# Kernel tuning notes

Hardware: AMD Instinct MI355X
Metric: run time of the kernel (lower is better)

The kernel has to match this reference:

```python
import jax, jax.numpy as jnp
import numpy as np

NUM_HEADS = 4

def setup_inputs() -> dict:
    key = jax.random.key(0)
    ks = jax.random.split(key, 8)
    B, C, H, W = 4, 256, 128, 128
    Cq = C // 8  # query/key channels
    x  = jax.random.normal(ks[0], (B, C, H, W), dtype=jnp.float32)
    Wq = jax.random.normal(ks[1], (Cq, C), dtype=jnp.float32) * 0.05
    bq = jax.random.normal(ks[2], (Cq,),  dtype=jnp.float32) * 0.01
    Wk = jax.random.normal(ks[3], (Cq, C), dtype=jnp.float32) * 0.05
    bk = jax.random.normal(ks[4], (Cq,),  dtype=jnp.float32) * 0.01
    Wv = jax.random.normal(ks[5], (C, C),  dtype=jnp.float32) * 0.05
    bv = jax.random.normal(ks[6], (C,),   dtype=jnp.float32) * 0.01
    # torch init is zeros; use a nonzero value so the attention path contributes
    gamma = jnp.array([0.5], dtype=jnp.float32)
    return {"x": x, "Wq": Wq, "bq": bq, "Wk": Wk, "bk": bk, "Wv": Wv, "bv": bv, "gamma": gamma}

def _conv1x1(x, Wm, b):
    # 1x1 conv == per-pixel linear map over channels
    return jnp.einsum('bchw,oc->bohw', x, Wm) + b[None, :, None, None]

def reference(x, Wq, bq, Wk, bk, Wv, bv, gamma):
    B, C, H, W = x.shape
    nh = NUM_HEADS
    # project, then fold heads into batch: (B*nh, c_head, H, W)
    q = _conv1x1(x, Wq, bq).reshape(B * nh, -1, H, W)
    k = _conv1x1(x, Wk, bk).reshape(B * nh, -1, H, W)
    v = _conv1x1(x, Wv, bv).reshape(B * nh, -1, H, W)
    # horizontal (row-wise) attention over W: energy [BH, H, W, W]
    e_h = jnp.einsum('bchw,bchv->bhwv', q, k)
    a_h = jax.nn.softmax(e_h, axis=-1)
    o_h = jnp.einsum('bhwv,bchv->bchw', a_h, v)  # (BH, cv, H, W)
    # vertical (column-wise) attention over H: energy [BH, W, H, H]
    e_v = jnp.einsum('bchw,bcgw->bwhg', q, k)
    a_v = jax.nn.softmax(e_v, axis=-1)
    # original permutes back as (BH, cv, W, H); requires H == W to add
    o_v = jnp.einsum('bwhg,bcgw->bcwh', a_v, v)
    attn = (o_h + o_v).reshape(B, C, H, W)
    return gamma * attn + x
```

## Files before the change

### kernel.cpp

```cpp
#include <hip/hip_runtime.h>

#define HW 16384

typedef __attribute__((ext_vector_type(8))) short short8;
typedef __attribute__((ext_vector_type(16))) float floatx16;
typedef __attribute__((ext_vector_type(4))) unsigned int uvec4;

__device__ inline unsigned short f2bf(float f) {
    unsigned u = __builtin_bit_cast(unsigned, f);
    u = (u + 0x7FFFu + ((u >> 16) & 1u)) >> 16;
    return (unsigned short)u;
}

__device__ inline unsigned pack_bf_trunc(float lo, float hi) {
    return __builtin_amdgcn_perm(__builtin_bit_cast(unsigned, hi),
                                 __builtin_bit_cast(unsigned, lo), 0x07060302u);
}

__global__ __launch_bounds__(256) void cast_xt_kernel(
    const float* __restrict__ x,
    const float* __restrict__ Wq, const float* __restrict__ Wk,
    const float* __restrict__ Wv, unsigned short* __restrict__ Wb,
    unsigned short* __restrict__ xt)
{
    __shared__ unsigned short T[64][66];
    const int tid = threadIdx.x;
    const int p0 = blockIdx.x * 64;
    const int c0 = blockIdx.y * 64;
    const int b  = blockIdx.z;

    if (b == 0 && blockIdx.y == 0 && blockIdx.x < 80) {
        int e0 = (blockIdx.x * 256 + tid) * 4;
        int row = e0 >> 8, col = e0 & 255;
        const float* src = (row < 32) ? (Wq + row * 256 + col)
                         : (row < 64) ? (Wk + (row - 32) * 256 + col)
                                      : (Wv + (row - 64) * 256 + col);
        float4 v = *(const float4*)src;
        if (row < 32) {
            const float L2E = 1.4426950408889634f;
            v.x *= L2E; v.y *= L2E; v.z *= L2E; v.w *= L2E;
        }
        uint2 pk;
        pk.x = f2bf(v.x) | ((unsigned)f2bf(v.y) << 16);
        pk.y = f2bf(v.z) | ((unsigned)f2bf(v.w) << 16);
        *(uint2*)&Wb[e0] = pk;
    }

    #pragma unroll
    for (int i = 0; i < 4; i++) {
        int e = i * 256 + tid;
        int c = e >> 4, seg = e & 15;
        float4 v = *(const float4*)&x[((b * 256 + c0 + c) << 14) + p0 + seg * 4];
        ((unsigned*)&T[c][seg * 4])[0] = f2bf(v.x) | ((unsigned)f2bf(v.y) << 16);
        ((unsigned*)&T[c][seg * 4])[1] = f2bf(v.z) | ((unsigned)f2bf(v.w) << 16);
    }
    __syncthreads();
    #pragma unroll
    for (int i = 0; i < 2; i++) {
        int e = i * 256 + tid;
        int p = e >> 3, cs = e & 7;
        unsigned short t[8];
        #pragma unroll
        for (int j = 0; j < 8; j++) t[j] = T[cs * 8 + j][p];
        uint4 pk;
        pk.x = t[0] | ((unsigned)t[1] << 16);
        pk.y = t[2] | ((unsigned)t[3] << 16);
        pk.z = t[4] | ((unsigned)t[5] << 16);
        pk.w = t[6] | ((unsigned)t[7] << 16);
        *(uint4*)&xt[(((b << 14) + p0 + p) << 8) + c0 + cs * 8] = pk;
    }
}

__global__ __launch_bounds__(256, 3) void proj_mfma_kernel(
    const unsigned short* __restrict__ Wb, const unsigned short* __restrict__ xt,
    const float* __restrict__ bq, const float* __restrict__ bk,
    const float* __restrict__ bv,
    unsigned short* __restrict__ qb, unsigned short* __restrict__ kb,
    unsigned short* __restrict__ vb)
{
    __shared__ __align__(16) unsigned short As[64 * 64];
    __shared__ __align__(16) unsigned short Bs[256 * 64];
    __shared__ float biasS[64];
    const int tid = threadIdx.x;
    const int logical = (blockIdx.x & 7) * 160 + (blockIdx.x >> 3);
    const int y5 = logical % 5;
    const int pb = logical / 5;
    const int p0  = (pb & 63) * 256;
    const int oc0 = y5 * 64;
    const int b   = pb >> 6;
    const int w = tid >> 6, lr = tid & 31, lh = (tid & 63) >> 5;

    if (tid < 64) biasS[tid] = (oc0 == 0)
        ? ((tid < 32) ? bq[tid] * 1.4426950408889634f : bk[tid - 32])
        : bv[oc0 - 64 + tid];

    floatx16 z16 = {0,0,0,0,0,0,0,0,0,0,0,0,0,0,0,0};
    floatx16 acc[2][2] = {{z16, z16}, {z16, z16}};
    const int bpx = (b << 14) + p0;

    for (int kc = 0; kc < 256; kc += 64) {
        if (kc) __syncthreads();
        #pragma unroll
        for (int i = 0; i < 2; i++) {
            int e = i * 256 + tid;
            int row = e >> 3, seg = e & 7, cp = seg ^ (row & 7);
            *(uint4*)&As[row * 64 + cp * 8] =
                *(const uint4*)&Wb[(oc0 + row) * 256 + kc + seg * 8];
        }
        #pragma unroll
        for (int i = 0; i < 8; i++) {
            int e = i * 256 + tid;
            int row = e >> 3, seg = e & 7, cp = seg ^ (row & 7);
            *(uint4*)&Bs[row * 64 + cp * 8] =
                *(const uint4*)&xt[((bpx + row) << 8) + kc + seg * 8];
        }
        __syncthreads();
        #pragma unroll
        for (int ks = 0; ks < 4; ks++) {
            int c = 2 * ks + lh;
            int cx = (c ^ (lr & 7)) * 8;
            short8 af0 = *(const short8*)&As[lr * 64 + cx];
            short8 af1 = *(const short8*)&As[(32 + lr) * 64 + cx];
            short8 bf0 = *(const short8*)&Bs[(64 * w + lr) * 64 + cx];
            short8 bf1 = *(const short8*)&Bs[(64 * w + 32 + lr) * 64 + cx];
            acc[0][0] = __builtin_amdgcn_mfma_f32_32x32x16_bf16(af0, bf0, acc[0][0], 0, 0, 0);
            acc[0][1] = __builtin_amdgcn_mfma_f32_32x32x16_bf16(af0, bf1, acc[0][1], 0, 0, 0);
            acc[1][0] = __builtin_amdgcn_mfma_f32_32x32x16_bf16(af1, bf0, acc[1][0], 0, 0, 0);
            acc[1][1] = __builtin_amdgcn_mfma_f32_32x32x16_bf16(af1, bf1, acc[1][1], 0, 0, 0);
        }
    }

    __syncthreads();
    if (oc0 == 0) {
        unsigned short* Cq = Bs;
        #pragma unroll
        for (int i = 0; i < 2; i++) {
            #pragma unroll
            for (int j = 0; j < 2; j++) {
                int px = 64 * w + 32 * j + lr;
                #pragma unroll
                for (int g = 0; g < 4; g++) {
                    float v0 = acc[i][j][4*g+0] + biasS[32*i + 8*g + 4*lh + 0];
                    float v1 = acc[i][j][4*g+1] + biasS[32*i + 8*g + 4*lh + 1];
                    float v2 = acc[i][j][4*g+2] + biasS[32*i + 8*g + 4*lh + 2];
                    float v3 = acc[i][j][4*g+3] + biasS[32*i + 8*g + 4*lh + 3];
                    uint2 u; u.x = pack_bf_trunc(v0, v1); u.y = pack_bf_trunc(v2, v3);
                    int cp = (4 * i + g) ^ (px & 7);
                    *(uint2*)&Cq[px * 64 + cp * 8 + 4 * lh] = u;
                }
            }
        }
        __syncthreads();
        #pragma unroll
        for (int i = 0; i < 8; i++) {
            int px = tid;
            int cp = i ^ (px & 7);
            uint4 val = *(const uint4*)&Cq[px * 64 + cp * 8];
            if (i < 4) *(uint4*)&qb[(unsigned)((b * 4 + i)     * HW + p0 + px) * 8] = val;
            else       *(uint4*)&kb[(unsigned)((b * 4 + i - 4) * HW + p0 + px) * 8] = val;
        }
    } else {
        unsigned short* Cv = Bs;
        #pragma unroll
        for (int i = 0; i < 2; i++) {
            #pragma unroll
            for (int j = 0; j < 2; j++) {
                int px = 64 * w + 32 * j + lr;
                #pragma unroll
                for (int reg = 0; reg < 16; reg++) {
                    int oc = 32 * i + (reg & 3) + 8 * (reg >> 2) + 4 * lh;
                    float v = acc[i][j][reg] + biasS[oc];
                    int cp = (px >> 3) ^ (oc & 31);
                    Cv[oc * 256 + cp * 8 + (px & 7)] =
                        (unsigned short)(__builtin_bit_cast(unsigned, v) >> 16);
                }
            }
        }
        __syncthreads();
        #pragma unroll
        for (int i = 0; i < 8; i++) {
            int u = i * 256 + tid;
            int oc = u >> 5, seg = u & 31;
            int cp = seg ^ (oc & 31);
            uint4 val = *(const uint4*)&Cv[oc * 256 + cp * 8];
            *(uint4*)&vb[(unsigned)(b * 256 + oc0 - 64 + oc) * HW + p0 + seg * 8] = val;
        }
    }
}

__global__ __launch_bounds__(256) void tv_kernel(
    const unsigned short* __restrict__ vb, unsigned short* __restrict__ vt)
{
    __shared__ unsigned short T[64][66];
    const int plane = blockIdx.y;
    const int tile  = blockIdx.x;
    const int tx = tile & 1, ty = tile >> 1;
    const unsigned* src = (const unsigned*)(vb + plane * HW);
    unsigned*       dst = (unsigned*)(vt + plane * HW);
    const int tid = threadIdx.x;
    #pragma unroll
    for (int i = 0; i < 8; i++) {
        int e = i * 256 + tid;
        int r = e >> 5, cp = e & 31;
        *(unsigned*)&T[r][2 * cp] = src[(ty * 64 + r) * 64 + tx * 32 + cp];
    }
    __syncthreads();
    #pragma unroll
    for (int i = 0; i < 8; i++) {
        int e = i * 256 + tid;
        int c = e >> 5, rp = e & 31;
        unsigned lo = T[2 * rp][c], hi = T[2 * rp + 1][c];
        dst[(tx * 64 + c) * 64 + ty * 32 + rp] = lo | (hi << 16);
    }
}

__global__ __launch_bounds__(256, 2) void attn_kernel(
    const unsigned short* __restrict__ qb, const unsigned short* __restrict__ kb,
    const unsigned short* __restrict__ vb,
    const unsigned short* __restrict__ vt,
    const float* __restrict__ xin, const float* __restrict__ gamma,
    float* __restrict__ out)
{
    __shared__ __align__(16) unsigned short Vs[2][64 * 128];

    const int tid = threadIdx.x;
    const int logical = (blockIdx.x & 7) * 256 + (blockIdx.x >> 3);
    const int y = logical & 127, bh = logical >> 7;
    const int w = tid >> 6, l = tid & 63, lr = l & 31, lh = l >> 5;

    #pragma unroll
    for (int s = 0; s < 2; s++) {
        const unsigned short* vsrc = s ? vt : vb;
        #pragma unroll
        for (int i = 0; i < 4; i++) {
            int e = i * 256 + tid;
            int ch = e >> 4, sg = e & 15, sgp = sg ^ (ch & 15);
            *(uint4*)&Vs[s][ch * 128 + sgp * 8] =
                *(const uint4*)(vsrc + (bh * 64 + ch) * HW + y * 128 + sg * 8);
        }
    }
    __syncthreads();

    floatx16 z16 = {0,0,0,0,0,0,0,0,0,0,0,0,0,0,0,0};
    floatx16 oh0 = z16, oh1 = z16;
    floatx16 ov0 = z16, ov1 = z16;
    short8 z8 = {0,0,0,0,0,0,0,0};
    float ssA = 1.0f, ssB = 1.0f;

    const unsigned short* qpl = qb + bh * (HW * 8);
    const unsigned short* kpl = kb + bh * (HW * 8);

    #pragma unroll
    for (int stage = 0; stage < 2; stage++) {
        short8 bf = z8;
        if (lh == 0) {
            int px = 32 * w + lr;
            int off = stage ? (px * 128 + y) : (y * 128 + px);
            bf = *(const short8*)(qpl + off * 8);
        }

        floatx16 et[4];
        #pragma unroll
        for (int kg = 0; kg < 4; kg++) {
            short8 af = z8;
            if (lh == 0) {
                int px = 32 * kg + lr;
                int off = stage ? (px * 128 + y) : (y * 128 + px);
                af = *(const short8*)(kpl + off * 8);
            }
            et[kg] = __builtin_amdgcn_mfma_f32_32x32x16_bf16(af, bf, z16, 0, 0, 0);
        }

        float partial = 0.f;
        #pragma unroll
        for (int kg = 0; kg < 4; kg++) {
            floatx16 e = et[kg];
            #pragma unroll
            for (int r = 0; r < 16; r++) {
                float p = exp2f(e[r]);
                e[r] = p;
                partial += p;
            }
            #pragma unroll
            for (int cc = 0; cc < 2; cc++) {
                unsigned X0 = pack_bf_trunc(e[8*cc+0], e[8*cc+1]);
                unsigned X1 = pack_bf_trunc(e[8*cc+2], e[8*cc+3]);
                unsigned X2 = pack_bf_trunc(e[8*cc+4], e[8*cc+5]);
                unsigned X3 = pack_bf_trunc(e[8*cc+6], e[8*cc+7]);
                unsigned pX0 = __shfl_xor(X0, 32);
                unsigned pX1 = __shfl_xor(X1, 32);
                unsigned pX2 = __shfl_xor(X2, 32);
                unsigned pX3 = __shfl_xor(X3, 32);
                uvec4 t;
                t.x = lh ? pX2 : X0;
                t.y = lh ? pX3 : X1;
                t.z = lh ? X2  : pX0;
                t.w = lh ? X3  : pX1;
                short8 pf = __builtin_bit_cast(short8, t);
                int ks = 2 * kg + cc;
                int cp = ((2 * ks + lh) ^ (lr & 15)) * 8;
                short8 v0 = *(const short8*)&Vs[stage][lr * 128 + cp];
                short8 v1 = *(const short8*)&Vs[stage][(32 + lr) * 128 + cp];
                if (stage == 0) {
                    oh0 = __builtin_amdgcn_mfma_f32_32x32x16_bf16(v0, pf, oh0, 0, 0, 0);
                    oh1 = __builtin_amdgcn_mfma_f32_32x32x16_bf16(v1, pf, oh1, 0, 0, 0);
                } else {
                    ov0 = __builtin_amdgcn_mfma_f32_32x32x16_bf16(v0, pf, ov0, 0, 0, 0);
                    ov1 = __builtin_amdgcn_mfma_f32_32x32x16_bf16(v1, pf, ov1, 0, 0, 0);
                }
            }
        }
        float ssum = partial + __shfl_xor(partial, 32);
        if (stage == 0) ssA = ssum; else ssB = ssum;
    }

    __syncthreads();

    const float g  = gamma[0];
    const float g0 = g / ssA, g1 = g / ssB;
    const int xq = 32 * w + lr;
    #pragma unroll
    for (int reg = 0; reg < 16; reg++) {
        int ch = (reg & 3) + 8 * (reg >> 2) + 4 * lh;
        int idx0 = (bh * 64 + ch) * HW + y * 128 + xq;
        int idx1 = (bh * 64 + 32 + ch) * HW + y * 128 + xq;
        out[idx0] = g0 * oh0[reg] + g1 * ov0[reg] + xin[idx0];
        out[idx1] = g0 * oh1[reg] + g1 * ov1[reg] + xin[idx1];
    }
}

extern "C" void kernel_launch(void* const* d_in, const int* in_sizes, int n_in,
                              void* d_out, int out_size, void* d_ws, size_t ws_size,
                              hipStream_t stream) {
    const float* x     = (const float*)d_in[0];
    const float* Wq    = (const float*)d_in[1];
    const float* bq    = (const float*)d_in[2];
    const float* Wk    = (const float*)d_in[3];
    const float* bk    = (const float*)d_in[4];
    const float* Wv    = (const float*)d_in[5];
    const float* bv    = (const float*)d_in[6];
    const float* gamma = (const float*)d_in[7];
    float* out = (float*)d_out;

    unsigned short* Wb   = (unsigned short*)d_ws;
    unsigned short* qb16 = Wb + 320 * 256;
    unsigned short* kb16 = qb16 + 16 * HW * 8;
    unsigned short* qt16 = kb16 + 16 * HW * 8;
    unsigned short* kt16 = qt16 + 16 * HW * 8;
    unsigned short* vb16 = kt16 + 16 * HW * 8;
    unsigned short* vt16 = vb16 + 1024 * HW;
    unsigned short* xt = (unsigned short*)d_out;
    (void)qt16; (void)kt16;

    cast_xt_kernel<<<dim3(256, 4, 4), 256, 0, stream>>>(x, Wq, Wk, Wv, Wb, xt);
    proj_mfma_kernel<<<dim3(1280), 256, 0, stream>>>(Wb, xt, bq, bk, bv, qb16, kb16, vb16);
    tv_kernel<<<dim3(4, 1024), 256, 0, stream>>>(vb16, vt16);
    attn_kernel<<<dim3(2048), 256, 0, stream>>>(qb16, kb16, vb16, vt16, x, gamma, out);
}
```

Measured before the change: 199.8 us.

## Fuse QKV projection and transpose into attention kernel, recomputing per row/column

After: 249.3 us. 24.8% more time.

```diff
diff --git a/kernel.cpp b/kernel.cpp
--- a/kernel.cpp
+++ b/kernel.cpp
@@ -15,6 +15,10 @@
 __device__ inline unsigned pack_bf_trunc(float lo, float hi) {
     return __builtin_amdgcn_perm(__builtin_bit_cast(unsigned, hi),
                                  __builtin_bit_cast(unsigned, lo), 0x07060302u);
+}
+
+__device__ inline unsigned short trunc_bf(float f) {
+    return (unsigned short)(__builtin_bit_cast(unsigned, f) >> 16);
 }
 
 __global__ __launch_bounds__(256) void cast_xt_kernel(
@@ -71,210 +75,105 @@
     }
 }
 
-__global__ __launch_bounds__(256, 3) void proj_mfma_kernel(
+__global__ __launch_bounds__(256, 2) void fused_kernel(
     const unsigned short* __restrict__ Wb, const unsigned short* __restrict__ xt,
     const float* __restrict__ bq, const float* __restrict__ bk,
     const float* __restrict__ bv,
-    unsigned short* __restrict__ qb, unsigned short* __restrict__ kb,
-    unsigned short* __restrict__ vb)
-{
-    __shared__ __align__(16) unsigned short As[64 * 64];
-    __shared__ __align__(16) unsigned short Bs[256 * 64];
-    __shared__ float biasS[64];
-    const int tid = threadIdx.x;
-    const int logical = (blockIdx.x & 7) * 160 + (blockIdx.x >> 3);
-    const int y5 = logical % 5;
-    const int pb = logical / 5;
-    const int p0  = (pb & 63) * 256;
-    const int oc0 = y5 * 64;
-    const int b   = pb >> 6;
-    const int w = tid >> 6, lr = tid & 31, lh = (tid & 63) >> 5;
-
-    if (tid < 64) biasS[tid] = (oc0 == 0)
-        ? ((tid < 32) ? bq[tid] * 1.4426950408889634f : bk[tid - 32])
-        : bv[oc0 - 64 + tid];
-
-    floatx16 z16 = {0,0,0,0,0,0,0,0,0,0,0,0,0,0,0,0};
-    floatx16 acc[2][2] = {{z16, z16}, {z16, z16}};
-    const int bpx = (b << 14) + p0;
-
-    for (int kc = 0; kc < 256; kc += 64) {
-        if (kc) __syncthreads();
-        #pragma unroll
-        for (int i = 0; i < 2; i++) {
-            int e = i * 256 + tid;
-            int row = e >> 3, seg = e & 7, cp = seg ^ (row & 7);
-            *(uint4*)&As[row * 64 + cp * 8] =
-                *(const uint4*)&Wb[(oc0 + row) * 256 + kc + seg * 8];
-        }
-        #pragma unroll
-        for (int i = 0; i < 8; i++) {
-            int e = i * 256 + tid;
-            int row = e >> 3, seg = e & 7, cp = seg ^ (row & 7);
-            *(uint4*)&Bs[row * 64 + cp * 8] =
-                *(const uint4*)&xt[((bpx + row) << 8) + kc + seg * 8];
-        }
-        __syncthreads();
-        #pragma unroll
-        for (int ks = 0; ks < 4; ks++) {
-            int c = 2 * ks + lh;
-            int cx = (c ^ (lr & 7)) * 8;
-            short8 af0 = *(const short8*)&As[lr * 64 + cx];
-            short8 af1 = *(const short8*)&As[(32 + lr) * 64 + cx];
-            short8 bf0 = *(const short8*)&Bs[(64 * w + lr) * 64 + cx];
-            short8 bf1 = *(const short8*)&Bs[(64 * w + 32 + lr) * 64 + cx];
-            acc[0][0] = __builtin_amdgcn_mfma_f32_32x32x16_bf16(af0, bf0, acc[0][0], 0, 0, 0);
-            acc[0][1] = __builtin_amdgcn_mfma_f32_32x32x16_bf16(af0, bf1, acc[0][1], 0, 0, 0);
-            acc[1][0] = __builtin_amdgcn_mfma_f32_32x32x16_bf16(af1, bf0, acc[1][0], 0, 0, 0);
-            acc[1][1] = __builtin_amdgcn_mfma_f32_32x32x16_bf16(af1, bf1, acc[1][1], 0, 0, 0);
-        }
-    }
-
-    __syncthreads();
-    if (oc0 == 0) {
-        unsigned short* Cq = Bs;
-        #pragma unroll
-        for (int i = 0; i < 2; i++) {
-            #pragma unroll
-            for (int j = 0; j < 2; j++) {
-                int px = 64 * w + 32 * j + lr;
-                #pragma unroll
-                for (int g = 0; g < 4; g++) {
-                    float v0 = acc[i][j][4*g+0] + biasS[32*i + 8*g + 4*lh + 0];
-                    float v1 = acc[i][j][4*g+1] + biasS[32*i + 8*g + 4*lh + 1];
-                    float v2 = acc[i][j][4*g+2] + biasS[32*i + 8*g + 4*lh + 2];
-                    float v3 = acc[i][j][4*g+3] + biasS[32*i + 8*g + 4*lh + 3];
-                    uint2 u; u.x = pack_bf_trunc(v0, v1); u.y = pack_bf_trunc(v2, v3);
-                    int cp = (4 * i + g) ^ (px & 7);
-                    *(uint2*)&Cq[px * 64 + cp * 8 + 4 * lh] = u;
-                }
-            }
-        }
-        __syncthreads();
-        #pragma unroll
-        for (int i = 0; i < 8; i++) {
-            int px = tid;
-            int cp = i ^ (px & 7);
-            uint4 val = *(const uint4*)&Cq[px * 64 + cp * 8];
-            if (i < 4) *(uint4*)&qb[(unsigned)((b * 4 + i)     * HW + p0 + px) * 8] = val;
-            else       *(uint4*)&kb[(unsigned)((b * 4 + i - 4) * HW + p0 + px) * 8] = val;
-        }
-    } else {
-        unsigned short* Cv = Bs;
-        #pragma unroll
-        for (int i = 0; i < 2; i++) {
-            #pragma unroll
-            for (int j = 0; j < 2; j++) {
-                int px = 64 * w + 32 * j + lr;
-                #pragma unroll
-                for (int reg = 0; reg < 16; reg++) {
-                    int oc = 32 * i + (reg & 3) + 8 * (reg >> 2) + 4 * lh;
-                    float v = acc[i][j][reg] + biasS[oc];
-                    int cp = (px >> 3) ^ (oc & 31);
-                    Cv[oc * 256 + cp * 8 + (px & 7)] =
-                        (unsigned short)(__builtin_bit_cast(unsigned, v) >> 16);
-                }
-            }
-        }
-        __syncthreads();
-        #pragma unroll
-        for (int i = 0; i < 8; i++) {
-            int u = i * 256 + tid;
-            int oc = u >> 5, seg = u & 31;
-            int cp = seg ^ (oc & 31);
-            uint4 val = *(const uint4*)&Cv[oc * 256 + cp * 8];
-            *(uint4*)&vb[(unsigned)(b * 256 + oc0 - 64 + oc) * HW + p0 + seg * 8] = val;
-        }
-    }
-}
-
-__global__ __launch_bounds__(256) void tv_kernel(
-    const unsigned short* __restrict__ vb, unsigned short* __restrict__ vt)
-{
-    __shared__ unsigned short T[64][66];
-    const int plane = blockIdx.y;
-    const int tile  = blockIdx.x;
-    const int tx = tile & 1, ty = tile >> 1;
-    const unsigned* src = (const unsigned*)(vb + plane * HW);
-    unsigned*       dst = (unsigned*)(vt + plane * HW);
-    const int tid = threadIdx.x;
-    #pragma unroll
-    for (int i = 0; i < 8; i++) {
-        int e = i * 256 + tid;
-        int r = e >> 5, cp = e & 31;
-        *(unsigned*)&T[r][2 * cp] = src[(ty * 64 + r) * 64 + tx * 32 + cp];
-    }
-    __syncthreads();
-    #pragma unroll
-    for (int i = 0; i < 8; i++) {
-        int e = i * 256 + tid;
-        int c = e >> 5, rp = e & 31;
-        unsigned lo = T[2 * rp][c], hi = T[2 * rp + 1][c];
-        dst[(tx * 64 + c) * 64 + ty * 32 + rp] = lo | (hi << 16);
-    }
-}
-
-__global__ __launch_bounds__(256, 2) void attn_kernel(
-    const unsigned short* __restrict__ qb, const unsigned short* __restrict__ kb,
-    const unsigned short* __restrict__ vb,
-    const unsigned short* __restrict__ vt,
     const float* __restrict__ xin, const float* __restrict__ gamma,
     float* __restrict__ out)
 {
+    __shared__ __align__(16) unsigned short XTS[128 * 64];
     __shared__ __align__(16) unsigned short Vs[2][64 * 128];
+    __shared__ __align__(16) unsigned short Kl[128 * 8];
+    __shared__ float biasS[80];
 
     const int tid = threadIdx.x;
-    const int logical = (blockIdx.x & 7) * 256 + (blockIdx.x >> 3);
-    const int y = logical & 127, bh = logical >> 7;
+    const int y = blockIdx.x >> 4, bh = blockIdx.x & 15;
+    const int b = bh >> 2, h = bh & 3;
     const int w = tid >> 6, l = tid & 63, lr = l & 31, lh = l >> 5;
-
-    #pragma unroll
-    for (int s = 0; s < 2; s++) {
-        const unsigned short* vsrc = s ? vt : vb;
-        #pragma unroll
-        for (int i = 0; i < 4; i++) {
-            int e = i * 256 + tid;
-            int ch = e >> 4, sg = e & 15, sgp = sg ^ (ch & 15);
-            *(uint4*)&Vs[s][ch * 128 + sgp * 8] =
-                *(const uint4*)(vsrc + (bh * 64 + ch) * HW + y * 128 + sg * 8);
-        }
-    }
-    __syncthreads();
+    const int px = 32 * w + lr;
+
+    if (tid < 80) biasS[tid] = (tid < 8)  ? bq[h * 8 + tid] * 1.4426950408889634f
+                             : (tid < 16) ? bk[h * 8 + tid - 8]
+                                          : bv[h * 64 + tid - 16];
+
+    const int wr0 = (lr < 8)  ? h * 8 + lr
+                  : (lr < 16) ? 32 + h * 8 + (lr - 8)
+                              : 64 + h * 64 + (lr - 16);
+    const int wr1 = 64 + h * 64 + 16 + lr;
+    const int wr2 = 64 + h * 64 + 48 + (lr & 15);
 
     floatx16 z16 = {0,0,0,0,0,0,0,0,0,0,0,0,0,0,0,0};
-    floatx16 oh0 = z16, oh1 = z16;
-    floatx16 ov0 = z16, ov1 = z16;
     short8 z8 = {0,0,0,0,0,0,0,0};
+    floatx16 oh0 = z16, oh1 = z16, ov0 = z16, ov1 = z16;
     float ssA = 1.0f, ssB = 1.0f;
 
-    const unsigned short* qpl = qb + bh * (HW * 8);
-    const unsigned short* kpl = kb + bh * (HW * 8);
-
-    #pragma unroll
-    for (int stage = 0; stage < 2; stage++) {
-        short8 bf = z8;
+    #pragma unroll
+    for (int side = 0; side < 2; side++) {
+        floatx16 a0 = z16, a1 = z16, a2 = z16;
+        for (int kc = 0; kc < 4; kc++) {
+            __syncthreads();
+            #pragma unroll
+            for (int i = 0; i < 4; i++) {
+                int e = i * 256 + tid;
+                int row = e >> 3, seg = e & 7, cp = seg ^ (row & 7);
+                int p = side ? (row * 128 + y) : (y * 128 + row);
+                *(uint4*)&XTS[row * 64 + cp * 8] =
+                    *(const uint4*)&xt[(((b << 14) + p) << 8) + kc * 64 + seg * 8];
+            }
+            __syncthreads();
+            #pragma unroll
+            for (int ks = 0; ks < 4; ks++) {
+                int cx = ((2 * ks + lh) ^ (lr & 7)) * 8;
+                short8 bfr = *(const short8*)&XTS[px * 64 + cx];
+                int ck = kc * 64 + (2 * ks + lh) * 8;
+                short8 af0 = *(const short8*)&Wb[wr0 * 256 + ck];
+                short8 af1 = *(const short8*)&Wb[wr1 * 256 + ck];
+                short8 af2 = *(const short8*)&Wb[wr2 * 256 + ck];
+                a0 = __builtin_amdgcn_mfma_f32_32x32x16_bf16(af0, bfr, a0, 0, 0, 0);
+                a1 = __builtin_amdgcn_mfma_f32_32x32x16_bf16(af1, bfr, a1, 0, 0, 0);
+                a2 = __builtin_amdgcn_mfma_f32_32x32x16_bf16(af2, bfr, a2, 0, 0, 0);
+            }
+        }
+        unsigned X0 = pack_bf_trunc(a0[0] + biasS[4 * lh + 0], a0[1] + biasS[4 * lh + 1]);
+        unsigned X1 = pack_bf_trunc(a0[2] + biasS[4 * lh + 2], a0[3] + biasS[4 * lh + 3]);
+        unsigned pX0 = __shfl_xor(X0, 32), pX1 = __shfl_xor(X1, 32);
+        short8 bfq = z8;
         if (lh == 0) {
-            int px = 32 * w + lr;
-            int off = stage ? (px * 128 + y) : (y * 128 + px);
-            bf = *(const short8*)(qpl + off * 8);
-        }
-
-        floatx16 et[4];
+            uvec4 t; t.x = X0; t.y = X1; t.z = pX0; t.w = pX1;
+            bfq = __builtin_bit_cast(short8, t);
+        }
+        {
+            uint2 kk;
+            kk.x = pack_bf_trunc(a0[4] + biasS[8 + 4 * lh + 0], a0[5] + biasS[8 + 4 * lh + 1]);
+            kk.y = pack_bf_trunc(a0[6] + biasS[8 + 4 * lh + 2], a0[7] + biasS[8 + 4 * lh + 3]);
+            *(uint2*)&Kl[px * 8 + 4 * lh] = kk;
+        }
+        #pragma unroll
+        for (int reg = 8; reg < 16; reg++) {
+            int ch = (reg & 3) + 8 * ((reg >> 2) - 2) + 4 * lh;
+            Vs[side][ch * 128 + (((px >> 3) ^ (ch & 15)) << 3) + (px & 7)] =
+                trunc_bf(a0[reg] + biasS[16 + ch]);
+        }
+        #pragma unroll
+        for (int reg = 0; reg < 16; reg++) {
+            int ch = 16 + (reg & 3) + 8 * (reg >> 2) + 4 * lh;
+            Vs[side][ch * 128 + (((px >> 3) ^ (ch & 15)) << 3) + (px & 7)] =
+                trunc_bf(a1[reg] + biasS[16 + ch]);
+        }
+        #pragma unroll
+        for (int reg = 0; reg < 8; reg++) {
+            int ch = 48 + (reg & 3) + 8 * (reg >> 2) + 4 * lh;
+            Vs[side][ch * 128 + (((px >> 3) ^ (ch & 15)) << 3) + (px & 7)] =
+                trunc_bf(a2[reg] + biasS[16 + ch]);
+        }
+        __syncthreads();
+        float partial = 0.f;
         #pragma unroll
         for (int kg = 0; kg < 4; kg++) {
             short8 af = z8;
-            if (lh == 0) {
-                int px = 32 * kg + lr;
-                int off = stage ? (px * 128 + y) : (y * 128 + px);
-                af = *(const short8*)(kpl + off * 8);
-            }
-            et[kg] = __builtin_amdgcn_mfma_f32_32x32x16_bf16(af, bf, z16, 0, 0, 0);
-        }
-
-        float partial = 0.f;
-        #pragma unroll
-        for (int kg = 0; kg < 4; kg++) {
-            floatx16 e = et[kg];
+            if (lh == 0) af = *(const short8*)&Kl[(32 * kg + lr) * 8];
+            floatx16 e = __builtin_amdgcn_mfma_f32_32x32x16_bf16(af, bfq, z16, 0, 0, 0);
             #pragma unroll
             for (int r = 0; r < 16; r++) {
                 float p = exp2f(e[r]);
@@ -283,25 +182,25 @@
             }
             #pragma unroll
             for (int cc = 0; cc < 2; cc++) {
-                unsigned X0 = pack_bf_trunc(e[8*cc+0], e[8*cc+1]);
-                unsigned X1 = pack_bf_trunc(e[8*cc+2], e[8*cc+3]);
-                unsigned X2 = pack_bf_trunc(e[8*cc+4], e[8*cc+5]);
-                unsigned X3 = pack_bf_trunc(e[8*cc+6], e[8*cc+7]);
-                unsigned pX0 = __shfl_xor(X0, 32);
-                unsigned pX1 = __shfl_xor(X1, 32);
-                unsigned pX2 = __shfl_xor(X2, 32);
-                unsigned pX3 = __shfl_xor(X3, 32);
+                unsigned Y0 = pack_bf_trunc(e[8*cc+0], e[8*cc+1]);
+                unsigned Y1 = pack_bf_trunc(e[8*cc+2], e[8*cc+3]);
+                unsigned Y2 = pack_bf_trunc(e[8*cc+4], e[8*cc+5]);
+                unsigned Y3 = pack_bf_trunc(e[8*cc+6], e[8*cc+7]);
+                unsigned pY0 = __shfl_xor(Y0, 32);
+                unsigned pY1 = __shfl_xor(Y1, 32);
+                unsigned pY2 = __shfl_xor(Y2, 32);
+                unsigned pY3 = __shfl_xor(Y3, 32);
                 uvec4 t;
-                t.x = lh ? pX2 : X0;
-                t.y = lh ? pX3 : X1;
-                t.z = lh ? X2  : pX0;
-                t.w = lh ? X3  : pX1;
+                t.x = lh ? pY2 : Y0;
+                t.y = lh ? pY3 : Y1;
+                t.z = lh ? Y2  : pY0;
+                t.w = lh ? Y3  : pY1;
                 short8 pf = __builtin_bit_cast(short8, t);
                 int ks = 2 * kg + cc;
                 int cp = ((2 * ks + lh) ^ (lr & 15)) * 8;
-                short8 v0 = *(const short8*)&Vs[stage][lr * 128 + cp];
-                short8 v1 = *(const short8*)&Vs[stage][(32 + lr) * 128 + cp];
-                if (stage == 0) {
+                short8 v0 = *(const short8*)&Vs[side][lr * 128 + cp];
+                short8 v1 = *(const short8*)&Vs[side][(32 + lr) * 128 + cp];
+                if (side == 0) {
                     oh0 = __builtin_amdgcn_mfma_f32_32x32x16_bf16(v0, pf, oh0, 0, 0, 0);
                     oh1 = __builtin_amdgcn_mfma_f32_32x32x16_bf16(v1, pf, oh1, 0, 0, 0);
                 } else {
@@ -311,19 +210,18 @@
             }
         }
         float ssum = partial + __shfl_xor(partial, 32);
-        if (stage == 0) ssA = ssum; else ssB = ssum;
+        if (side == 0) ssA = ssum; else ssB = ssum;
     }
 
     __syncthreads();
 
     const float g  = gamma[0];
     const float g0 = g / ssA, g1 = g / ssB;
-    const int xq = 32 * w + lr;
     #pragma unroll
     for (int reg = 0; reg < 16; reg++) {
         int ch = (reg & 3) + 8 * (reg >> 2) + 4 * lh;
-        int idx0 = (bh * 64 + ch) * HW + y * 128 + xq;
-        int idx1 = (bh * 64 + 32 + ch) * HW + y * 128 + xq;
+        int idx0 = (bh * 64 + ch) * HW + y * 128 + px;
+        int idx1 = (bh * 64 + 32 + ch) * HW + y * 128 + px;
         out[idx0] = g0 * oh0[reg] + g1 * ov0[reg] + xin[idx0];
         out[idx1] = g0 * oh1[reg] + g1 * ov1[reg] + xin[idx1];
     }
@@ -342,18 +240,9 @@
     const float* gamma = (const float*)d_in[7];
     float* out = (float*)d_out;
 
-    unsigned short* Wb   = (unsigned short*)d_ws;
-    unsigned short* qb16 = Wb + 320 * 256;
-    unsigned short* kb16 = qb16 + 16 * HW * 8;
-    unsigned short* qt16 = kb16 + 16 * HW * 8;
-    unsigned short* kt16 = qt16 + 16 * HW * 8;
-    unsigned short* vb16 = kt16 + 16 * HW * 8;
-    unsigned short* vt16 = vb16 + 1024 * HW;
-    unsigned short* xt = (unsigned short*)d_out;
-    (void)qt16; (void)kt16;
+    unsigned short* Wb = (unsigned short*)d_ws;
+    unsigned short* xt = Wb + 320 * 256;
 
     cast_xt_kernel<<<dim3(256, 4, 4), 256, 0, stream>>>(x, Wq, Wk, Wv, Wb, xt);
-    proj_mfma_kernel<<<dim3(1280), 256, 0, stream>>>(Wb, xt, bq, bk, bv, qb16, kb16, vb16);
-    tv_kernel<<<dim3(4, 1024), 256, 0, stream>>>(vb16, vt16);
-    attn_kernel<<<dim3(2048), 256, 0, stream>>>(qb16, kb16, vb16, vt16, x, gamma, out);
-}
+    fused_kernel<<<dim3(2048), 256, 0, stream>>>(Wb, xt, bq, bk, bv, x, gamma, out);
+}
```
